# Kernel tuning notes

Measured on AMD Instinct MI355X. Metric: run time of the kernel, lower is better.

Reference implementation:

```python
import jax, jax.numpy as jnp
import numpy as np

B, S, I, H = 64, 512, 256, 256


def setup_inputs() -> dict:
    key = jax.random.key(0)
    ks = jax.random.split(key, 24)
    d = {
        "inputs": jax.random.normal(ks[0], (B, S, I), jnp.float32),
        "timestamps": jax.random.uniform(ks[1], (B, S), jnp.float32) * 10.0,
    }
    names = ["Wi", "Ui", "Wf", "Uf", "Wo", "Uo", "Wc", "Uc", "Wd"]
    dims = [(I, H), (H, H), (I, H), (H, H), (I, H), (H, H), (I, H), (H, H), (H, H)]
    for idx, (n, (din, dout)) in enumerate(zip(names, dims)):
        kw, kb = ks[2 + 2 * idx], ks[3 + 2 * idx]
        bound = 1.0 / np.sqrt(din)
        d[n + "_w"] = jax.random.uniform(kw, (dout, din), jnp.float32, -bound, bound)
        d[n + "_b"] = jax.random.uniform(kb, (dout,), jnp.float32, -bound, bound)
    # extra nn.Parameter biases, initialized to zeros as in the torch module
    for n in ["bi", "bf", "bo", "bc", "bd"]:
        d[n] = jnp.zeros((H,), jnp.float32)
    return d


def reference(inputs, timestamps,
              Wi_w, Wi_b, Ui_w, Ui_b, Wf_w, Wf_b, Uf_w, Uf_b,
              Wo_w, Wo_b, Uo_w, Uo_b, Wc_w, Wc_b, Uc_w, Uc_b,
              Wd_w, Wd_b, bi, bf, bo, bc, bd):
    b, seq, _ = inputs.shape
    h_dim = Wi_w.shape[0]
    # time-decay factor T = 1/log(t + e)  (module uses literal 2.7183)
    T = 1.0 / jnp.log(timestamps + 2.7183)          # [B,S]
    # hoist input projections out of the recurrence (same math, W*x per step)
    Xi = jnp.einsum('bsi,hi->bsh', inputs, Wi_w) + Wi_b + bi
    Xf = jnp.einsum('bsi,hi->bsh', inputs, Wf_w) + Wf_b + bf
    Xo = jnp.einsum('bsi,hi->bsh', inputs, Wo_w) + Wo_b + bo
    Xc = jnp.einsum('bsi,hi->bsh', inputs, Wc_w) + Wc_b + bc
    xs = (Xi.transpose(1, 0, 2), Xf.transpose(1, 0, 2),
          Xo.transpose(1, 0, 2), Xc.transpose(1, 0, 2),
          T.T[:, :, None])                          # each [S,B,*]

    def step(carry, x):
        h, c = carry
        xi, xf, xo, xc, t = x
        C_ST = jnp.tanh(c @ Wd_w.T + Wd_b + bd)     # short-term memory
        c = c - C_ST + t * C_ST                     # decayed cell
        i = jax.nn.sigmoid(xi + h @ Ui_w.T + Ui_b)
        f = jax.nn.sigmoid(xf + h @ Uf_w.T + Uf_b)
        o = jax.nn.sigmoid(xo + h @ Uo_w.T + Uo_b)
        Cn = jnp.tanh(xc + h @ Uc_w.T + Uc_b)
        c = f * c + i * Cn
        h = o * jnp.tanh(c)
        return (h, c), (h, c)

    h0 = jnp.zeros((b, h_dim), inputs.dtype)
    c0 = jnp.zeros((b, h_dim), inputs.dtype)
    _, (hs, cs) = jax.lax.scan(step, (h0, c0), xs)
    outputs = hs.transpose(1, 0, 2)                 # [B,S,H]
    cell_states = cs.transpose(1, 0, 2)
    return outputs, (outputs, cell_states)
```

## Files before the change

kernel.cpp:

```cpp
#include <hip/hip_runtime.h>
#include <cstdint>
#include <cstddef>


#define B_   64
#define S_   512
#define H_   256
#define BSH_ ((size_t)B_ * S_ * H_)

typedef _Float16 f16;
typedef _Float16 f16x8 __attribute__((ext_vector_type(8)));
typedef short    s16x8 __attribute__((ext_vector_type(8)));
typedef float    f32x4 __attribute__((ext_vector_type(4)));
typedef unsigned int u32x4 __attribute__((ext_vector_type(4)));

static __device__ __forceinline__ unsigned short f32_to_bf16(float f) {
    union { float f; uint32_t u; } v; v.f = f;
    uint32_t u = v.u;
    u += 0x7fffu + ((u >> 16) & 1u);
    return (unsigned short)(u >> 16);
}

static __device__ __forceinline__ float sigm(float z) {
    return 1.0f / (1.0f + __expf(-z));
}
static __device__ __forceinline__ float tanh_fast(float z) {
    float e = __expf(-2.0f * fabsf(z));
    float t = (1.0f - e) / (1.0f + e);
    return z >= 0.0f ? t : -t;
}

__global__ void prep_w4(const float* __restrict__ Wi, const float* __restrict__ Wf,
                        const float* __restrict__ Wo, const float* __restrict__ Wc,
                        const float* __restrict__ Wib, const float* __restrict__ Wfb,
                        const float* __restrict__ Wob, const float* __restrict__ Wcb,
                        const float* __restrict__ Uib, const float* __restrict__ Ufb,
                        const float* __restrict__ Uob, const float* __restrict__ Ucb,
                        const float* __restrict__ bi,  const float* __restrict__ bf_,
                        const float* __restrict__ bo,  const float* __restrict__ bc,
                        unsigned short* __restrict__ W4, float* __restrict__ bias4) {
    const int n = blockIdx.x;
    const int k = threadIdx.x;
    const int g = n >> 8, o = n & 255;
    const float* W = (g == 0) ? Wi : (g == 1) ? Wf : (g == 2) ? Wo : Wc;
    W4[n * 256 + k] = f32_to_bf16(W[o * 256 + k]);
    if (k == 0) {
        const float* wb = (g == 0) ? Wib : (g == 1) ? Wfb : (g == 2) ? Wob : Wcb;
        const float* ub = (g == 0) ? Uib : (g == 1) ? Ufb : (g == 2) ? Uob : Ucb;
        const float* sb = (g == 0) ? bi  : (g == 1) ? bf_ : (g == 2) ? bo  : bc;
        bias4[n] = wb[o] + ub[o] + sb[o];
    }
}

__global__ void prep_wfrag(const float* __restrict__ Ui, const float* __restrict__ Uf,
                           const float* __restrict__ Uo, const float* __restrict__ Uc,
                           const float* __restrict__ Wd, uint4* __restrict__ wfg) {
    const int id = blockIdx.x * 256 + threadIdx.x;
    const int l  = id & 63;
    const int ks = (id >> 6) & 7;
    const int t  = (id >> 9) & 1;
    const int qg = id >> 10;
    const int q  = qg / 5;
    const int g  = qg - q * 5;
    const float* U = (g == 0) ? Ui : (g == 1) ? Uf : (g == 2) ? Uo : (g == 3) ? Uc : Wd;
    const int row = 32 * q + t * 16 + (l & 15);
    const int k0  = 32 * ks + (l >> 4) * 8;
    const float* src = U + (size_t)row * 256 + k0;
    union { f16 h[8]; uint4 v; } pk;
    #pragma unroll
    for (int i = 0; i < 8; ++i) pk.h[i] = (f16)src[i];
    wfg[id] = pk.v;
}

__global__ void prep_T(const float* __restrict__ tsp, float* __restrict__ Tm1) {
    const int i = blockIdx.x * 256 + threadIdx.x;
    Tm1[i] = 1.0f / logf(tsp[i] + 2.7183f) - 1.0f;
}

__global__ void prep_zero(unsigned int* __restrict__ p, int n) {
    const int i = blockIdx.x * 256 + threadIdx.x;
    if (i < n) p[i] = 0u;
}

__global__ __launch_bounds__(256) void proj_gemm(const float* __restrict__ X,
        const unsigned short* __restrict__ W4, const float* __restrict__ bias4,
        f16* __restrict__ Xbuf) {
    __shared__ __align__(16) unsigned short a_s[64 * 40];
    __shared__ __align__(16) unsigned short b_s[64 * 40];
    const int bid = blockIdx.x;
    const int m0 = (bid >> 4) * 64;
    const int n0 = (bid & 15) * 64;
    const int tid  = threadIdx.x;
    const int lane = tid & 63;
    const int w    = tid >> 6;
    const int srow = tid >> 2;
    const int scol = (tid & 3) * 8;
    const int r  = lane & 15;
    const int kg = lane >> 4;

    f32x4 acc[4] = {{0,0,0,0},{0,0,0,0},{0,0,0,0},{0,0,0,0}};

    for (int kt = 0; kt < 8; ++kt) {
        const int k0 = kt * 32;
        float4 av0 = *reinterpret_cast<const float4*>(X + (size_t)(m0 + srow) * 256 + k0 + scol);
        float4 av1 = *reinterpret_cast<const float4*>(X + (size_t)(m0 + srow) * 256 + k0 + scol + 4);
        union { unsigned short us[8]; uint4 v; } pk;
        pk.us[0] = f32_to_bf16(av0.x); pk.us[1] = f32_to_bf16(av0.y);
        pk.us[2] = f32_to_bf16(av0.z); pk.us[3] = f32_to_bf16(av0.w);
        pk.us[4] = f32_to_bf16(av1.x); pk.us[5] = f32_to_bf16(av1.y);
        pk.us[6] = f32_to_bf16(av1.z); pk.us[7] = f32_to_bf16(av1.w);
        *reinterpret_cast<uint4*>(a_s + srow * 40 + scol) = pk.v;
        uint4 bv = *reinterpret_cast<const uint4*>(W4 + (size_t)(n0 + srow) * 256 + k0 + scol);
        *reinterpret_cast<uint4*>(b_s + srow * 40 + scol) = bv;
        __syncthreads();

        s16x8 af = *reinterpret_cast<const s16x8*>(a_s + (w * 16 + r) * 40 + kg * 8);
        #pragma unroll
        for (int nt = 0; nt < 4; ++nt) {
            s16x8 bfr = *reinterpret_cast<const s16x8*>(b_s + (nt * 16 + r) * 40 + kg * 8);
            acc[nt] = __builtin_amdgcn_mfma_f32_16x16x32_bf16(af, bfr, acc[nt], 0, 0, 0);
        }
        __syncthreads();
    }
    #pragma unroll
    for (int nt = 0; nt < 4; ++nt) {
        const int n = n0 + nt * 16 + r;
        const int gidx = n >> 8, jj = n & 255;
        const float bn = bias4[n];
        #pragma unroll
        for (int reg = 0; reg < 4; ++reg) {
            const int m = m0 + w * 16 + kg * 4 + reg;
            Xbuf[((size_t)m * 256 + jj) * 4 + gidx] = (f16)(acc[nt][reg] + bn);
        }
    }
}

__global__ __launch_bounds__(320) void recur(
        const uint4* __restrict__ wfg, const f16* __restrict__ Xbuf,
        const float* __restrict__ Wdb, const float* __restrict__ bdv,
        const float* __restrict__ Tm1,
        uint4* __restrict__ hxf, uint4* __restrict__ cxf,
        unsigned int* __restrict__ tags, float* __restrict__ out) {
    extern __shared__ __align__(16) char smemraw[];
    uint4* wfr  = (uint4*)smemraw;
    float* pre  = (float*)(wfr + 5120);
    f16*   stgh = (f16*)(pre + 16 * 164);
    f16*   stgc = stgh + 256;
    float* obh  = (float*)(stgc + 256);
    float* obc  = obh + 2048;

    const int tid = threadIdx.x;
    const int bid = blockIdx.x;
    const int G = bid & 7;
    const int q = bid >> 3;
    const int g = tid >> 6;
    const int l = tid & 63;

    {
        const uint4* src = wfg + (size_t)q * 5120;
        #pragma unroll
        for (int i = 0; i < 16; ++i) wfr[tid + i * 320] = src[tid + i * 320];
    }
    const int gb = tid >> 5;
    const int jl = tid & 31;
    const int j  = 32 * q + jl;
    float cj = 0.0f, bD = 0.0f;
    if (tid < 256) bD = Wdb[j] + bdv[j];
    __syncthreads();

    uint4* hxb = hxf + (size_t)G * 1024;
    uint4* cxb = cxf + (size_t)G * 1024;
    unsigned int* tg = tags + (size_t)G * 256;

    f16x8 A[8];
    #pragma unroll
    for (int p = 0; p < 8; ++p) A[p] = (f16x8)(f16)0;

    for (int s = 0; s < 512; ++s) {
        const int par = s & 1;

        uint2 xv = {0, 0};
        float tm1 = 0.f;
        if (tid < 256) {
            const size_t m = (size_t)(8 * G + gb) * 512 + s;
            xv  = *reinterpret_cast<const uint2*>(Xbuf + (m * 256 + j) * 4);
            tm1 = Tm1[m];
        }

        f32x4 acc0 = {0.f, 0.f, 0.f, 0.f};
        f32x4 acc1 = {0.f, 0.f, 0.f, 0.f};
        #pragma unroll
        for (int p = 0; p < 8; ++p) {
            f16x8 b0 = __builtin_bit_cast(f16x8, wfr[((g * 2 + 0) * 8 + p) * 64 + l]);
            f16x8 b1 = __builtin_bit_cast(f16x8, wfr[((g * 2 + 1) * 8 + p) * 64 + l]);
            acc0 = __builtin_amdgcn_mfma_f32_16x16x32_f16(A[p], b0, acc0, 0, 0, 0);
            acc1 = __builtin_amdgcn_mfma_f32_16x16x32_f16(A[p], b1, acc1, 0, 0, 0);
        }
        {
            const int mb = (l >> 4) * 4;
            const int c0 = g * 32 + (l & 15);
            #pragma unroll
            for (int reg = 0; reg < 4; ++reg) {
                pre[(mb + reg) * 164 + c0]      = acc0[reg];
                pre[(mb + reg) * 164 + c0 + 16] = acc1[reg];
            }
        }
        __syncthreads();

        if (tid < 256) {
            const float* pb = pre + gb * 164;
            const f16* xp = reinterpret_cast<const f16*>(&xv);
            float CST  = tanh_fast(pb[128 + jl] + bD);
            float cdec = cj + tm1 * CST;
            float ig = sigm((float)xp[0] + pb[jl]);
            float fg = sigm((float)xp[1] + pb[32 + jl]);
            float og = sigm((float)xp[2] + pb[64 + jl]);
            float Cn = tanh_fast((float)xp[3] + pb[96 + jl]);
            cj = fg * cdec + ig * Cn;
            float hn = og * tanh_fast(cj);
            obh[(s & 7) * 256 + tid] = hn;
            obc[(s & 7) * 256 + tid] = cj;
            stgh[tid] = (f16)hn;
            stgc[tid] = (f16)cj;
        }
        __syncthreads();

        if (s != 511) {
            if (g == 4) {
                const int lm = l & 31;
                const int kg = lm >> 3, b = lm & 7;
                const bool isC = l >= 32;
                u32x4 v = __builtin_bit_cast(u32x4, *reinterpret_cast<const uint4*>(
                    (isC ? stgc : stgh) + b * 32 + kg * 8));
                uint4* pp = (isC ? cxb : hxb) + par * 512 + q * 64 + kg * 16 + b;
                asm volatile("global_store_dwordx4 %0, %1, off sc0 sc1"
                             :: "v"(pp), "v"(v) : "memory");
                asm volatile("s_waitcnt vmcnt(0)" ::: "memory");
                if (l == 0) {
                    unsigned int* tp = tg + par * 128 + q * 16;
                    unsigned tv = (unsigned)(s + 1);
                    asm volatile("global_store_dword %0, %1, off sc0 sc1"
                                 :: "v"(tp), "v"(tv) : "memory");
                }
            }
        }
        if ((s & 7) == 7 && tid < 256) {
            #pragma unroll
            for (int sf = 0; sf < 8; ++sf) {
                const size_t mm = (size_t)(8 * G + gb) * 512 + (s - 7 + sf);
                const size_t oi = mm * 256 + j;
                float hv = obh[sf * 256 + tid];
                float cv = obc[sf * 256 + tid];
                out[oi] = hv; out[BSH_ + oi] = hv; out[2 * BSH_ + oi] = cv;
            }
        }
        if (s != 511) {
            {
                const unsigned tgt = (unsigned)(s + 1);
                const unsigned int* tp = tg + par * 128 + (l & 7) * 16;
                unsigned v; int spins = 0;
                for (;;) {
                    asm volatile("global_load_dword %0, %1, off sc0 sc1\n\t"
                                 "s_waitcnt vmcnt(0)"
                                 : "=v"(v) : "v"(tp) : "memory");
                    if (__all((int)(v >= tgt))) break;
                    if (++spins > (1 << 18)) break;
                    __builtin_amdgcn_s_sleep(1);
                }
            }
            {
                const uint4* base0 = ((g == 4) ? cxb : hxb) + par * 512 + l;
                const uint4* base1 = base0 + 256;
                u32x4 r0, r1, r2, r3, r4, r5, r6, r7;
                asm volatile(
                    "global_load_dwordx4 %0, %8, off sc0 sc1\n\t"
                    "global_load_dwordx4 %1, %8, off offset:1024 sc0 sc1\n\t"
                    "global_load_dwordx4 %2, %8, off offset:2048 sc0 sc1\n\t"
                    "global_load_dwordx4 %3, %8, off offset:3072 sc0 sc1\n\t"
                    "global_load_dwordx4 %4, %9, off sc0 sc1\n\t"
                    "global_load_dwordx4 %5, %9, off offset:1024 sc0 sc1\n\t"
                    "global_load_dwordx4 %6, %9, off offset:2048 sc0 sc1\n\t"
                    "global_load_dwordx4 %7, %9, off offset:3072 sc0 sc1\n\t"
                    "s_waitcnt vmcnt(0)"
                    : "=&v"(r0), "=&v"(r1), "=&v"(r2), "=&v"(r3),
                      "=&v"(r4), "=&v"(r5), "=&v"(r6), "=&v"(r7)
                    : "v"(base0), "v"(base1)
                    : "memory");
                A[0] = __builtin_bit_cast(f16x8, r0);
                A[1] = __builtin_bit_cast(f16x8, r1);
                A[2] = __builtin_bit_cast(f16x8, r2);
                A[3] = __builtin_bit_cast(f16x8, r3);
                A[4] = __builtin_bit_cast(f16x8, r4);
                A[5] = __builtin_bit_cast(f16x8, r5);
                A[6] = __builtin_bit_cast(f16x8, r6);
                A[7] = __builtin_bit_cast(f16x8, r7);
            }
        }
    }
}

extern "C" void kernel_launch(void* const* d_in, const int* in_sizes, int n_in,
                              void* d_out, int out_size, void* d_ws, size_t ws_size,
                              hipStream_t stream) {
    const float* inputs = (const float*)d_in[0];
    const float* tsp    = (const float*)d_in[1];
    const float* Wi_w = (const float*)d_in[2],  * Wi_b = (const float*)d_in[3];
    const float* Ui_w = (const float*)d_in[4],  * Ui_b = (const float*)d_in[5];
    const float* Wf_w = (const float*)d_in[6],  * Wf_b = (const float*)d_in[7];
    const float* Uf_w = (const float*)d_in[8],  * Uf_b = (const float*)d_in[9];
    const float* Wo_w = (const float*)d_in[10], * Wo_b = (const float*)d_in[11];
    const float* Uo_w = (const float*)d_in[12], * Uo_b = (const float*)d_in[13];
    const float* Wc_w = (const float*)d_in[14], * Wc_b = (const float*)d_in[15];
    const float* Uc_w = (const float*)d_in[16], * Uc_b = (const float*)d_in[17];
    const float* Wd_w = (const float*)d_in[18], * Wd_b = (const float*)d_in[19];
    const float* bi = (const float*)d_in[20], * bf_ = (const float*)d_in[21];
    const float* bo = (const float*)d_in[22], * bc  = (const float*)d_in[23];
    const float* bd = (const float*)d_in[24];

    char* ws = (char*)d_ws;
    f16*            Xbuf  = (f16*)ws;
    unsigned short* W4    = (unsigned short*)(ws + 67108864);
    float*          bias4 = (float*)(ws + 67633152);
    uint4*          wfg   = (uint4*)(ws + 67637248);
    uint4*          hxf   = (uint4*)(ws + 68292608);
    uint4*          cxf   = (uint4*)(ws + 68423680);
    unsigned int*   tags  = (unsigned int*)(ws + 68554752);
    float*          Tm1   = (float*)(ws + 68562944);

    prep_w4<<<1024, 256, 0, stream>>>(Wi_w, Wf_w, Wo_w, Wc_w,
                                      Wi_b, Wf_b, Wo_b, Wc_b,
                                      Ui_b, Uf_b, Uo_b, Uc_b,
                                      bi, bf_, bo, bc, W4, bias4);
    prep_wfrag<<<160, 256, 0, stream>>>(Ui_w, Uf_w, Uo_w, Uc_w, Wd_w, wfg);
    prep_T<<<128, 256, 0, stream>>>(tsp, Tm1);
    prep_zero<<<264, 256, 0, stream>>>((unsigned int*)hxf, 67584);
    proj_gemm<<<8192, 256, 0, stream>>>(inputs, W4, bias4, Xbuf);

    const size_t lds_bytes = 5120 * 16 + 16 * 164 * 4
                           + 2 * 256 * 2 + 2 * 2048 * 4;
    recur<<<64, 320, lds_bytes, stream>>>(wfg, Xbuf, Wd_b, bd, Tm1,
                                          hxf, cxf, tags, (float*)d_out);
}
```

Baseline: 1.561 ms.

## Interleave two batch sub-groups per block to hide cross-block h/c exchange latency

The recurrence kernel now runs on half as many blocks, and each block handles two independent batch sub-groups (A and B) with separate exchange buffers and tags. While the other blocks are still publishing and polling for one sub-group's hidden and cell state, the block runs the MFMA and gate work for the other sub-group. The aim is to cover the global-memory handshake latency that serialised each timestep. In exchange, each block does twice the per-step work and uses more LDS. Only half the blocks now occupy CUs, so per-step compute time may grow.

```diff
diff --git a/kernel.cpp b/kernel.cpp
--- a/kernel.cpp
+++ b/kernel.cpp
@@ -139,20 +139,26 @@
         const uint4* __restrict__ wfg, const f16* __restrict__ Xbuf,
         const float* __restrict__ Wdb, const float* __restrict__ bdv,
         const float* __restrict__ Tm1,
-        uint4* __restrict__ hxf, uint4* __restrict__ cxf,
-        unsigned int* __restrict__ tags, float* __restrict__ out) {
+        uint4* __restrict__ hxA, uint4* __restrict__ cxA,
+        uint4* __restrict__ hxB, uint4* __restrict__ cxB,
+        unsigned int* __restrict__ tagsA, unsigned int* __restrict__ tagsB,
+        float* __restrict__ out) {
     extern __shared__ __align__(16) char smemraw[];
-    uint4* wfr  = (uint4*)smemraw;
-    float* pre  = (float*)(wfr + 5120);
-    f16*   stgh = (f16*)(pre + 16 * 164);
-    f16*   stgc = stgh + 256;
-    float* obh  = (float*)(stgc + 256);
-    float* obc  = obh + 2048;
+    uint4* wfr   = (uint4*)smemraw;
+    float* pre   = (float*)(wfr + 5120);
+    f16*   stgAh = (f16*)(pre + 16 * 164);
+    f16*   stgAc = stgAh + 256;
+    f16*   stgBh = stgAc + 256;
+    f16*   stgBc = stgBh + 256;
+    float* obhA  = (float*)(stgBc + 256);
+    float* obcA  = obhA + 2048;
+    float* obhB  = obcA + 2048;
+    float* obcB  = obhB + 2048;
 
     const int tid = threadIdx.x;
     const int bid = blockIdx.x;
-    const int G = bid & 7;
-    const int q = bid >> 3;
+    const int G = bid & 3;
+    const int q = bid >> 2;
     const int g = tid >> 6;
     const int l = tid & 63;
 
@@ -164,139 +170,197 @@
     const int gb = tid >> 5;
     const int jl = tid & 31;
     const int j  = 32 * q + jl;
-    float cj = 0.0f, bD = 0.0f;
+    float cjA = 0.0f, cjB = 0.0f, bD = 0.0f;
     if (tid < 256) bD = Wdb[j] + bdv[j];
     __syncthreads();
 
-    uint4* hxb = hxf + (size_t)G * 1024;
-    uint4* cxb = cxf + (size_t)G * 1024;
-    unsigned int* tg = tags + (size_t)G * 256;
-
-    f16x8 A[8];
+    uint4* hxbA = hxA + (size_t)G * 1024;
+    uint4* cxbA = cxA + (size_t)G * 1024;
+    uint4* hxbB = hxB + (size_t)G * 1024;
+    uint4* cxbB = cxB + (size_t)G * 1024;
+    unsigned int* tgA = tagsA + (size_t)G * 256;
+    unsigned int* tgB = tagsB + (size_t)G * 256;
+
+    f16x8 A8[8], B8[8];
     #pragma unroll
-    for (int p = 0; p < 8; ++p) A[p] = (f16x8)(f16)0;
+    for (int p = 0; p < 8; ++p) { A8[p] = (f16x8)(f16)0; B8[p] = (f16x8)(f16)0; }
+
+#define POLL_TAGS(TGPTR, TGT)                                                \
+    {                                                                        \
+        const unsigned int* tp_ = (TGPTR) + (l & 7) * 16;                    \
+        unsigned v_; int spins_ = 0;                                         \
+        for (;;) {                                                           \
+            asm volatile("global_load_dword %0, %1, off sc0 sc1\n\t"         \
+                         "s_waitcnt vmcnt(0)"                                \
+                         : "=v"(v_) : "v"(tp_) : "memory");                  \
+            if (__all((int)(v_ >= (unsigned)(TGT)))) break;                  \
+            if (++spins_ > (1 << 18)) break;                                 \
+            __builtin_amdgcn_s_sleep(1);                                     \
+        }                                                                    \
+    }
+
+#define GATHER8(DST, BASEPTR)                                                \
+    {                                                                        \
+        const uint4* b0_ = (BASEPTR);                                        \
+        const uint4* b1_ = b0_ + 256;                                        \
+        u32x4 r0_, r1_, r2_, r3_, r4_, r5_, r6_, r7_;                        \
+        asm volatile(                                                        \
+            "global_load_dwordx4 %0, %8, off sc0 sc1\n\t"                    \
+            "global_load_dwordx4 %1, %8, off offset:1024 sc0 sc1\n\t"        \
+            "global_load_dwordx4 %2, %8, off offset:2048 sc0 sc1\n\t"        \
+            "global_load_dwordx4 %3, %8, off offset:3072 sc0 sc1\n\t"        \
+            "global_load_dwordx4 %4, %9, off sc0 sc1\n\t"                    \
+            "global_load_dwordx4 %5, %9, off offset:1024 sc0 sc1\n\t"        \
+            "global_load_dwordx4 %6, %9, off offset:2048 sc0 sc1\n\t"        \
+            "global_load_dwordx4 %7, %9, off offset:3072 sc0 sc1\n\t"        \
+            "s_waitcnt vmcnt(0)"                                             \
+            : "=&v"(r0_), "=&v"(r1_), "=&v"(r2_), "=&v"(r3_),                \
+              "=&v"(r4_), "=&v"(r5_), "=&v"(r6_), "=&v"(r7_)                 \
+            : "v"(b0_), "v"(b1_)                                             \
+            : "memory");                                                     \
+        DST[0] = __builtin_bit_cast(f16x8, r0_);                             \
+        DST[1] = __builtin_bit_cast(f16x8, r1_);                             \
+        DST[2] = __builtin_bit_cast(f16x8, r2_);                             \
+        DST[3] = __builtin_bit_cast(f16x8, r3_);                             \
+        DST[4] = __builtin_bit_cast(f16x8, r4_);                             \
+        DST[5] = __builtin_bit_cast(f16x8, r5_);                             \
+        DST[6] = __builtin_bit_cast(f16x8, r6_);                             \
+        DST[7] = __builtin_bit_cast(f16x8, r7_);                             \
+    }
+
+#define PUBLISH64(STGH, STGC, HX, CX, PAR)                                   \
+    {                                                                        \
+        const int lm_ = l & 31;                                              \
+        const int kg_ = lm_ >> 3, b_ = lm_ & 7;                              \
+        const bool isC_ = l >= 32;                                           \
+        u32x4 v_ = __builtin_bit_cast(u32x4, *reinterpret_cast<const uint4*>(\
+            (isC_ ? (STGC) : (STGH)) + b_ * 32 + kg_ * 8));                  \
+        uint4* pp_ = (isC_ ? (CX) : (HX)) + (PAR) * 512 + q * 64 + kg_ * 16 + b_; \
+        asm volatile("global_store_dwordx4 %0, %1, off sc0 sc1"              \
+                     :: "v"(pp_), "v"(v_) : "memory");                       \
+    }
+
+#define MFMA_PASS(SRC)                                                       \
+    {                                                                        \
+        f32x4 acc0 = {0.f, 0.f, 0.f, 0.f};                                   \
+        f32x4 acc1 = {0.f, 0.f, 0.f, 0.f};                                   \
+        _Pragma("unroll")                                                    \
+        for (int p = 0; p < 8; ++p) {                                        \
+            f16x8 b0 = __builtin_bit_cast(f16x8, wfr[((g * 2 + 0) * 8 + p) * 64 + l]); \
+            f16x8 b1 = __builtin_bit_cast(f16x8, wfr[((g * 2 + 1) * 8 + p) * 64 + l]); \
+            acc0 = __builtin_amdgcn_mfma_f32_16x16x32_f16(SRC[p], b0, acc0, 0, 0, 0);  \
+            acc1 = __builtin_amdgcn_mfma_f32_16x16x32_f16(SRC[p], b1, acc1, 0, 0, 0);  \
+        }                                                                    \
+        const int mb_ = (l >> 4) * 4;                                        \
+        const int c0_ = g * 32 + (l & 15);                                   \
+        _Pragma("unroll")                                                    \
+        for (int reg = 0; reg < 4; ++reg) {                                  \
+            pre[(mb_ + reg) * 164 + c0_]      = acc0[reg];                   \
+            pre[(mb_ + reg) * 164 + c0_ + 16] = acc1[reg];                   \
+        }                                                                    \
+    }
+
+#define GATES(XV, TM, CJ, STGH, STGC, OBH, OBC)                              \
+    {                                                                        \
+        const float* pb_ = pre + gb * 164;                                   \
+        const f16* xp_ = reinterpret_cast<const f16*>(&(XV));                \
+        float CST_  = tanh_fast(pb_[128 + jl] + bD);                         \
+        float cdec_ = (CJ) + (TM) * CST_;                                    \
+        float ig_ = sigm((float)xp_[0] + pb_[jl]);                           \
+        float fg_ = sigm((float)xp_[1] + pb_[32 + jl]);                      \
+        float og_ = sigm((float)xp_[2] + pb_[64 + jl]);                      \
+        float Cn_ = tanh_fast((float)xp_[3] + pb_[96 + jl]);                 \
+        (CJ) = fg_ * cdec_ + ig_ * Cn_;                                      \
+        float hn_ = og_ * tanh_fast(CJ);                                     \
+        (OBH)[(s & 7) * 256 + tid] = hn_;                                    \
+        (OBC)[(s & 7) * 256 + tid] = (CJ);                                   \
+        (STGH)[tid] = (f16)hn_;                                              \
+        (STGC)[tid] = (f16)(CJ);                                             \
+    }
 
     for (int s = 0; s < 512; ++s) {
-        const int par = s & 1;
-
-        uint2 xv = {0, 0};
-        float tm1 = 0.f;
+        const int par  = s & 1;
+        const int parB = (s - 1) & 1;
+
+        uint2 xvA = {0, 0};
+        float tmA = 0.f;
         if (tid < 256) {
-            const size_t m = (size_t)(8 * G + gb) * 512 + s;
-            xv  = *reinterpret_cast<const uint2*>(Xbuf + (m * 256 + j) * 4);
-            tm1 = Tm1[m];
-        }
-
-        f32x4 acc0 = {0.f, 0.f, 0.f, 0.f};
-        f32x4 acc1 = {0.f, 0.f, 0.f, 0.f};
-        #pragma unroll
-        for (int p = 0; p < 8; ++p) {
-            f16x8 b0 = __builtin_bit_cast(f16x8, wfr[((g * 2 + 0) * 8 + p) * 64 + l]);
-            f16x8 b1 = __builtin_bit_cast(f16x8, wfr[((g * 2 + 1) * 8 + p) * 64 + l]);
-            acc0 = __builtin_amdgcn_mfma_f32_16x16x32_f16(A[p], b0, acc0, 0, 0, 0);
-            acc1 = __builtin_amdgcn_mfma_f32_16x16x32_f16(A[p], b1, acc1, 0, 0, 0);
-        }
-        {
-            const int mb = (l >> 4) * 4;
-            const int c0 = g * 32 + (l & 15);
-            #pragma unroll
-            for (int reg = 0; reg < 4; ++reg) {
-                pre[(mb + reg) * 164 + c0]      = acc0[reg];
-                pre[(mb + reg) * 164 + c0 + 16] = acc1[reg];
+            const size_t m = (size_t)(16 * G + gb) * 512 + s;
+            xvA = *reinterpret_cast<const uint2*>(Xbuf + (m * 256 + j) * 4);
+            tmA = Tm1[m];
+        }
+
+        MFMA_PASS(A8)
+        __syncthreads();
+        if (tid < 256) GATES(xvA, tmA, cjA, stgAh, stgAc, obhA, obcA)
+        __syncthreads();
+
+        if (g == 4 && s != 511) {
+            PUBLISH64(stgAh, stgAc, hxbA, cxbA, par)
+            asm volatile("s_waitcnt vmcnt(0)" ::: "memory");
+            if (l == 0) {
+                unsigned int* tp = tgA + par * 128 + q * 16;
+                unsigned tv = (unsigned)(s + 1);
+                asm volatile("global_store_dword %0, %1, off sc0 sc1"
+                             :: "v"(tp), "v"(tv) : "memory");
             }
         }
-        __syncthreads();
-
+        if (s > 0) {
+            POLL_TAGS(tgB + parB * 128, s)
+            GATHER8(B8, ((g == 4) ? cxbB : hxbB) + parB * 512 + l)
+        }
+
+        uint2 xvB = {0, 0};
+        float tmB = 0.f;
         if (tid < 256) {
-            const float* pb = pre + gb * 164;
-            const f16* xp = reinterpret_cast<const f16*>(&xv);
-            float CST  = tanh_fast(pb[128 + jl] + bD);
-            float cdec = cj + tm1 * CST;
-            float ig = sigm((float)xp[0] + pb[jl]);
-            float fg = sigm((float)xp[1] + pb[32 + jl]);
-            float og = sigm((float)xp[2] + pb[64 + jl]);
-            float Cn = tanh_fast((float)xp[3] + pb[96 + jl]);
-            cj = fg * cdec + ig * Cn;
-            float hn = og * tanh_fast(cj);
-            obh[(s & 7) * 256 + tid] = hn;
-            obc[(s & 7) * 256 + tid] = cj;
-            stgh[tid] = (f16)hn;
-            stgc[tid] = (f16)cj;
-        }
-        __syncthreads();
-
-        if (s != 511) {
-            if (g == 4) {
-                const int lm = l & 31;
-                const int kg = lm >> 3, b = lm & 7;
-                const bool isC = l >= 32;
-                u32x4 v = __builtin_bit_cast(u32x4, *reinterpret_cast<const uint4*>(
-                    (isC ? stgc : stgh) + b * 32 + kg * 8));
-                uint4* pp = (isC ? cxb : hxb) + par * 512 + q * 64 + kg * 16 + b;
-                asm volatile("global_store_dwordx4 %0, %1, off sc0 sc1"
-                             :: "v"(pp), "v"(v) : "memory");
-                asm volatile("s_waitcnt vmcnt(0)" ::: "memory");
-                if (l == 0) {
-                    unsigned int* tp = tg + par * 128 + q * 16;
-                    unsigned tv = (unsigned)(s + 1);
-                    asm volatile("global_store_dword %0, %1, off sc0 sc1"
-                                 :: "v"(tp), "v"(tv) : "memory");
-                }
-            }
-        }
+            const size_t m = (size_t)(16 * G + 8 + gb) * 512 + s;
+            xvB = *reinterpret_cast<const uint2*>(Xbuf + (m * 256 + j) * 4);
+            tmB = Tm1[m];
+        }
+
+        MFMA_PASS(B8)
+        __syncthreads();
+        if (tid < 256) GATES(xvB, tmB, cjB, stgBh, stgBc, obhB, obcB)
+        __syncthreads();
+
         if ((s & 7) == 7 && tid < 256) {
             #pragma unroll
             for (int sf = 0; sf < 8; ++sf) {
-                const size_t mm = (size_t)(8 * G + gb) * 512 + (s - 7 + sf);
-                const size_t oi = mm * 256 + j;
-                float hv = obh[sf * 256 + tid];
-                float cv = obc[sf * 256 + tid];
-                out[oi] = hv; out[BSH_ + oi] = hv; out[2 * BSH_ + oi] = cv;
+                const size_t mA = (size_t)(16 * G + gb) * 512 + (s - 7 + sf);
+                const size_t oiA = mA * 256 + j;
+                float hv = obhA[sf * 256 + tid];
+                float cv = obcA[sf * 256 + tid];
+                out[oiA] = hv; out[BSH_ + oiA] = hv; out[2 * BSH_ + oiA] = cv;
+                const size_t mB = (size_t)(16 * G + 8 + gb) * 512 + (s - 7 + sf);
+                const size_t oiB = mB * 256 + j;
+                hv = obhB[sf * 256 + tid];
+                cv = obcB[sf * 256 + tid];
+                out[oiB] = hv; out[BSH_ + oiB] = hv; out[2 * BSH_ + oiB] = cv;
             }
         }
+
+        if (g == 4 && s != 511) {
+            PUBLISH64(stgBh, stgBc, hxbB, cxbB, par)
+        }
         if (s != 511) {
-            {
-                const unsigned tgt = (unsigned)(s + 1);
-                const unsigned int* tp = tg + par * 128 + (l & 7) * 16;
-                unsigned v; int spins = 0;
-                for (;;) {
-                    asm volatile("global_load_dword %0, %1, off sc0 sc1\n\t"
-                                 "s_waitcnt vmcnt(0)"
-                                 : "=v"(v) : "v"(tp) : "memory");
-                    if (__all((int)(v >= tgt))) break;
-                    if (++spins > (1 << 18)) break;
-                    __builtin_amdgcn_s_sleep(1);
-                }
+            POLL_TAGS(tgA + par * 128, s + 1)
+            GATHER8(A8, ((g == 4) ? cxbA : hxbA) + par * 512 + l)
+        }
+        if (g == 4 && s != 511) {
+            asm volatile("s_waitcnt vmcnt(0)" ::: "memory");
+            if (l == 0) {
+                unsigned int* tp = tgB + par * 128 + q * 16;
+                unsigned tv = (unsigned)(s + 1);
+                asm volatile("global_store_dword %0, %1, off sc0 sc1"
+                             :: "v"(tp), "v"(tv) : "memory");
             }
-            {
-                const uint4* base0 = ((g == 4) ? cxb : hxb) + par * 512 + l;
-                const uint4* base1 = base0 + 256;
-                u32x4 r0, r1, r2, r3, r4, r5, r6, r7;
-                asm volatile(
-                    "global_load_dwordx4 %0, %8, off sc0 sc1\n\t"
-                    "global_load_dwordx4 %1, %8, off offset:1024 sc0 sc1\n\t"
-                    "global_load_dwordx4 %2, %8, off offset:2048 sc0 sc1\n\t"
-                    "global_load_dwordx4 %3, %8, off offset:3072 sc0 sc1\n\t"
-                    "global_load_dwordx4 %4, %9, off sc0 sc1\n\t"
-                    "global_load_dwordx4 %5, %9, off offset:1024 sc0 sc1\n\t"
-                    "global_load_dwordx4 %6, %9, off offset:2048 sc0 sc1\n\t"
-                    "global_load_dwordx4 %7, %9, off offset:3072 sc0 sc1\n\t"
-                    "s_waitcnt vmcnt(0)"
-                    : "=&v"(r0), "=&v"(r1), "=&v"(r2), "=&v"(r3),
-                      "=&v"(r4), "=&v"(r5), "=&v"(r6), "=&v"(r7)
-                    : "v"(base0), "v"(base1)
-                    : "memory");
-                A[0] = __builtin_bit_cast(f16x8, r0);
-                A[1] = __builtin_bit_cast(f16x8, r1);
-                A[2] = __builtin_bit_cast(f16x8, r2);
-                A[3] = __builtin_bit_cast(f16x8, r3);
-                A[4] = __builtin_bit_cast(f16x8, r4);
-                A[5] = __builtin_bit_cast(f16x8, r5);
-                A[6] = __builtin_bit_cast(f16x8, r6);
-                A[7] = __builtin_bit_cast(f16x8, r7);
-            }
-        }
-    }
+        }
+    }
+#undef POLL_TAGS
+#undef GATHER8
+#undef PUBLISH64
+#undef MFMA_PASS
+#undef GATES
 }
 
 extern "C" void kernel_launch(void* const* d_in, const int* in_sizes, int n_in,
@@ -322,9 +386,12 @@
     unsigned short* W4    = (unsigned short*)(ws + 67108864);
     float*          bias4 = (float*)(ws + 67633152);
     uint4*          wfg   = (uint4*)(ws + 67637248);
-    uint4*          hxf   = (uint4*)(ws + 68292608);
-    uint4*          cxf   = (uint4*)(ws + 68423680);
-    unsigned int*   tags  = (unsigned int*)(ws + 68554752);
+    uint4*          hxA   = (uint4*)(ws + 68292608);
+    uint4*          cxA   = (uint4*)(ws + 68358144);
+    uint4*          hxB   = (uint4*)(ws + 68423680);
+    uint4*          cxB   = (uint4*)(ws + 68489216);
+    unsigned int*   tagsA = (unsigned int*)(ws + 68554752);
+    unsigned int*   tagsB = (unsigned int*)(ws + 68558848);
     float*          Tm1   = (float*)(ws + 68562944);
 
     prep_w4<<<1024, 256, 0, stream>>>(Wi_w, Wf_w, Wo_w, Wc_w,
@@ -333,11 +400,12 @@
                                       bi, bf_, bo, bc, W4, bias4);
     prep_wfrag<<<160, 256, 0, stream>>>(Ui_w, Uf_w, Uo_w, Uc_w, Wd_w, wfg);
     prep_T<<<128, 256, 0, stream>>>(tsp, Tm1);
-    prep_zero<<<264, 256, 0, stream>>>((unsigned int*)hxf, 67584);
+    prep_zero<<<8, 256, 0, stream>>>(tagsA, 2048);
     proj_gemm<<<8192, 256, 0, stream>>>(inputs, W4, bias4, Xbuf);
 
     const size_t lds_bytes = 5120 * 16 + 16 * 164 * 4
-                           + 2 * 256 * 2 + 2 * 2048 * 4;
-    recur<<<64, 320, lds_bytes, stream>>>(wfg, Xbuf, Wd_b, bd, Tm1,
-                                          hxf, cxf, tags, (float*)d_out);
-}
+                           + 4 * 256 * 2 + 4 * 2048 * 4;
+    recur<<<32, 320, lds_bytes, stream>>>(wfg, Xbuf, Wd_b, bd, Tm1,
+                                          hxA, cxA, hxB, cxB,
+                                          tagsA, tagsB, (float*)d_out);
+}
```

Measured after the change: 2.132 ms. 36.6% more time.
